# Kernel tuning notes

Hardware: AMD Instinct MI355X
Metric: run time of the kernel (lower is better)

The kernel has to match this reference:

```python
import jax, jax.numpy as jnp
import numpy as np

B, C, N, V, W = 2, 4, 224, 7, 256
EMB, H = 256, 4
TOKEN_DIM = C * N           # 896
HF = int(C * 2.66)          # 10 (GDFN hidden features)
EPS_LN = 1e-6


def _dwconv3(x, w):
    # depthwise 3x3, padding=1; x:[B,Ch,Hh,Ww], w:[Ch,1,3,3]
    return jax.lax.conv_general_dilated(
        x, w, window_strides=(1, 1), padding='SAME',
        feature_group_count=x.shape[1],
        dimension_numbers=('NCHW', 'OIHW', 'NCHW'))


def _layernorm_c(x, g, b):
    # LayerNorm over channel dim (NCHW), eps=1e-6
    m = jnp.mean(x, axis=1, keepdims=True)
    v = jnp.mean((x - m) ** 2, axis=1, keepdims=True)
    return (x - m) / jnp.sqrt(v + EPS_LN) * g[None, :, None, None] + b[None, :, None, None]


def setup_inputs() -> dict:
    key = jax.random.key(0)
    ks = jax.random.split(key, 12)
    s = 0.02
    return {
        'buffer':     jax.random.normal(ks[0], (B, C, N, V, W), jnp.float32),
        'w_in':       jax.random.normal(ks[1], (EMB, TOKEN_DIM), jnp.float32) * s,
        'temperature': jnp.ones((1, H, 1, 1), jnp.float32),
        'ln1_g':      jnp.ones((EMB,), jnp.float32),
        'ln1_b':      jnp.zeros((EMB,), jnp.float32),
        'w_qkv':      jax.random.normal(ks[2], (3 * EMB, EMB), jnp.float32) * s,
        'w_qkv_dw':   jax.random.normal(ks[3], (3 * EMB, 1, 3, 3), jnp.float32) * s,
        'w_proj':     jax.random.normal(ks[4], (TOKEN_DIM, EMB), jnp.float32) * s,
        'w_attca':    jax.random.normal(ks[5], (2 * H, H), jnp.float32) * s,
        'ln2_g':      jnp.ones((C,), jnp.float32),
        'ln2_b':      jnp.zeros((C,), jnp.float32),
        'w_pin':      jax.random.normal(ks[6], (2 * HF, C), jnp.float32) * s,
        'w_dw':       jax.random.normal(ks[7], (2 * HF, 1, 3, 3), jnp.float32) * s,
        'w_pout':     jax.random.normal(ks[8], (C, HF), jnp.float32) * s,
    }


def reference(buffer, w_in, temperature, ln1_g, ln1_b, w_qkv, w_qkv_dw,
              w_proj, w_attca, ln2_g, ln2_b, w_pin, w_dw, w_pout):
    S = V * W
    d = EMB // H
    # b c n v w -> b (v w) (c n)
    x_tok = buffer.transpose(0, 3, 4, 1, 2).reshape(B, S, C * N)
    # b c n v w -> (b n) c v w
    x_res = buffer.transpose(0, 2, 1, 3, 4).reshape(B * N, C, V, W)

    x_tok = jnp.einsum('bsk,ek->bse', x_tok, w_in)                  # linear_in
    x = x_tok.reshape(B, V, W, EMB).transpose(0, 3, 1, 2)           # b emb v w
    x_norm = _layernorm_c(x, ln1_g, ln1_b)

    qkv = jnp.einsum('bchw,oc->bohw', x_norm, w_qkv)                # 1x1 conv
    qkv = _dwconv3(qkv, w_qkv_dw)
    q, k, v_ = jnp.split(qkv, 3, axis=1)

    def heads(t):  # b (h d) v w -> b h (v w) d
        return t.reshape(B, H, d, S).transpose(0, 1, 3, 2)
    q, k, v_ = heads(q), heads(k), heads(v_)

    # F.normalize(dim=-1), eps=1e-12
    q = q / jnp.maximum(jnp.linalg.norm(q, axis=-1, keepdims=True), 1e-12)
    k = k / jnp.maximum(jnp.linalg.norm(k, axis=-1, keepdims=True), 1e-12)

    attn_logits = jnp.einsum('bhid,bhjd->bhij', q, k) * temperature
    attn0 = jax.nn.softmax(attn_logits, axis=-1)
    attn1 = jnp.maximum(attn_logits, 0.0) ** 2
    attn1 = jax.nn.gelu(attn1, approximate=False) * attn1
    x_att = jnp.einsum('bhij,oh->boij', attn1, w_attca)             # 1x1 conv over heads
    scale, shift = jnp.split(x_att, 2, axis=1)
    attn = attn0 * (1.0 + scale) + shift

    out = jnp.einsum('bhij,bhjd->bhid', attn, v_)
    out = out.transpose(0, 1, 3, 2).reshape(B, EMB, V, W)           # b (h d) v w
    out = jnp.einsum('bchw,oc->bohw', out, w_proj)                  # proj to token_dim
    out = out.reshape(B, C, N, V, W).transpose(0, 2, 1, 3, 4).reshape(B * N, C, V, W)

    x2 = x_res + out
    epi = _layernorm_c(x2, ln2_g, ln2_b)
    # GDFN
    h_ = jnp.einsum('bchw,oc->bohw', epi, w_pin)
    h_ = _dwconv3(h_, w_dw)
    h1, h2 = jnp.split(h_, 2, axis=1)
    h_ = jax.nn.gelu(h1, approximate=False) * h2
    epi = jnp.einsum('bchw,oc->bohw', h_, w_pout)
    epi = x2 + epi

    return epi.reshape(B, N, C, V, W).transpose(0, 2, 1, 3, 4)      # b c n v w
```

## Files before the change

kernel.cpp:

```cpp
#include <hip/hip_runtime.h>
#include <math.h>

#define B_ 2
#define C_ 4
#define N_ 224
#define V_ 7
#define W_ 256
#define S_ 1792
#define EMB_ 256
#define H_ 4
#define D_ 64
#define TOK_ 896
#define HF_ 10
#define JC_ 4
#define JRANGE_ (S_ / JC_)
#define JSTEPS_ (JRANGE_ / 32)

typedef __attribute__((ext_vector_type(8))) short short8;
typedef __attribute__((ext_vector_type(4))) short bf16x4;
typedef __attribute__((ext_vector_type(4))) float f32x4;

#define MFMA16(a, b, c) __builtin_amdgcn_mfma_f32_16x16x32_bf16(a, b, c, 0, 0, 0)

__device__ inline short f2bf(float f) {
    union { float f; unsigned u; } x; x.f = f;
    unsigned u = x.u;
    unsigned r = (u + 0x7fffu + ((u >> 16) & 1u)) >> 16;
    return (short)r;
}
__device__ inline float bf2f(short s) {
    union { unsigned u; float f; } x;
    x.u = ((unsigned)(unsigned short)s) << 16;
    return x.f;
}

__global__ __launch_bounds__(256) void gemm_mfma_kernel(
    const float* __restrict__ A, const float* __restrict__ Bact, float* __restrict__ Cm,
    int M, int N, int K, long b_bs, long c_bs)
{
    Bact += (long)blockIdx.z * b_bs;
    Cm   += (long)blockIdx.z * c_bs;
    const int m0 = blockIdx.y * 128, n0 = blockIdx.x * 128;
    __shared__ __align__(16) short As[128][40];
    __shared__ __align__(16) short Bs[128][40];
    const int t = threadIdx.x;
    const int lane = t & 63;
    const int wave = t >> 6;
    const int wr = wave >> 1, wc = wave & 1;
    const int col = lane & 15, grp = lane >> 4;
    const int ar = t >> 3, ak = (t & 7) * 4;
    const int bn = t & 127, kb = (t >> 7) * 16;
    f32x4 acc[4][4];
    #pragma unroll
    for (int i = 0; i < 4; ++i)
        #pragma unroll
        for (int j = 0; j < 4; ++j) acc[i][j] = (f32x4){0.f, 0.f, 0.f, 0.f};
    for (int k0 = 0; k0 < K; k0 += 32) {
        #pragma unroll
        for (int p = 0; p < 4; ++p) {
            f32x4 v = *(const f32x4*)&A[(long)(m0 + ar + p * 32) * K + k0 + ak];
            bf16x4 pk;
            pk[0] = f2bf(v[0]); pk[1] = f2bf(v[1]); pk[2] = f2bf(v[2]); pk[3] = f2bf(v[3]);
            *(bf16x4*)&As[ar + p * 32][ak] = pk;
        }
        float tv[16];
        #pragma unroll
        for (int j = 0; j < 16; ++j)
            tv[j] = Bact[(long)(k0 + kb + j) * N + n0 + bn];
        short8 b0, b1;
        #pragma unroll
        for (int j = 0; j < 8; ++j) { b0[j] = f2bf(tv[j]); b1[j] = f2bf(tv[8 + j]); }
        *(short8*)&Bs[bn][kb]     = b0;
        *(short8*)&Bs[bn][kb + 8] = b1;
        __syncthreads();
        short8 af[4], bfr[4];
        #pragma unroll
        for (int m16 = 0; m16 < 4; ++m16)
            af[m16] = *(const short8*)&As[wr * 64 + m16 * 16 + col][grp * 8];
        #pragma unroll
        for (int n16 = 0; n16 < 4; ++n16)
            bfr[n16] = *(const short8*)&Bs[wc * 64 + n16 * 16 + col][grp * 8];
        #pragma unroll
        for (int m16 = 0; m16 < 4; ++m16)
            #pragma unroll
            for (int n16 = 0; n16 < 4; ++n16)
                acc[m16][n16] = MFMA16(af[m16], bfr[n16], acc[m16][n16]);
        __syncthreads();
    }
    #pragma unroll
    for (int m16 = 0; m16 < 4; ++m16)
        #pragma unroll
        for (int n16 = 0; n16 < 4; ++n16)
            #pragma unroll
            for (int r = 0; r < 4; ++r)
                Cm[(long)(m0 + wr * 64 + m16 * 16 + grp * 4 + r) * N
                   + n0 + wc * 64 + n16 * 16 + col] = acc[m16][n16][r];
}

__global__ __launch_bounds__(256) void ln1_kernel(
    const float* __restrict__ X, const float* __restrict__ g,
    const float* __restrict__ b, float* __restrict__ Y)
{
    int sl = threadIdx.x & 63, dg = threadIdx.x >> 6;
    int s = blockIdx.x * 64 + sl;
    int img = blockIdx.y;
    const float* xp = X + (long)img * EMB_ * S_ + s;
    float sum = 0.f, sq = 0.f;
    for (int c = dg * 64; c < dg * 64 + 64; ++c) {
        float v = xp[(long)c * S_];
        sum += v; sq += v * v;
    }
    __shared__ float rs[64][5], rq[64][5];
    rs[sl][dg] = sum; rq[sl][dg] = sq;
    __syncthreads();
    float tot = rs[sl][0] + rs[sl][1] + rs[sl][2] + rs[sl][3];
    float tq  = rq[sl][0] + rq[sl][1] + rq[sl][2] + rq[sl][3];
    float mean = tot * (1.f / EMB_);
    float var  = tq * (1.f / EMB_) - mean * mean;
    float inv  = rsqrtf(var + 1e-6f);
    float* yp = Y + (long)img * EMB_ * S_ + s;
    for (int c = dg * 64; c < dg * 64 + 64; ++c)
        yp[(long)c * S_] = (xp[(long)c * S_] - mean) * inv * g[c] + b[c];
}

__global__ void dwconv3_kernel(const float* __restrict__ X, const float* __restrict__ Wt,
                               float* __restrict__ Y, short* __restrict__ vbf,
                               long total, int Ch)
{
    long idx = (long)blockIdx.x * blockDim.x + threadIdx.x;
    long stride = (long)gridDim.x * blockDim.x;
    for (; idx < total; idx += stride) {
        int w = (int)(idx % W_);
        long t = idx / W_;
        int h = (int)(t % V_); t /= V_;
        int ch = (int)(t % Ch);
        long img_ch = idx / ((long)V_ * W_);
        const float* wp = Wt + ch * 9;
        const float* xp = X + img_ch * (V_ * W_);
        float acc = 0.f;
        #pragma unroll
        for (int dy = -1; dy <= 1; ++dy) {
            int h2 = h + dy;
            if (h2 < 0 || h2 >= V_) continue;
            #pragma unroll
            for (int dx = -1; dx <= 1; ++dx) {
                int w2 = w + dx;
                if (w2 < 0 || w2 >= W_) continue;
                acc += xp[h2 * W_ + w2] * wp[(dy + 1) * 3 + (dx + 1)];
            }
        }
        Y[idx] = acc;
        if (vbf && ch >= 512) {
            int b = (int)(t / Ch);
            vbf[((long)b * 256 + (ch - 512)) * S_ + h * W_ + w] = f2bf(acc);
        }
    }
}

__global__ __launch_bounds__(256) void headnorm_kernel(
    const float* __restrict__ qkvd, const float* __restrict__ temp,
    short* __restrict__ qn, short* __restrict__ kn)
{
    int s0 = blockIdx.x * 64;
    int bh = blockIdx.y; int b = bh >> 2, h = bh & 3;
    int isq = blockIdx.z;
    int ch0 = b * 768 + (isq ? 0 : EMB_) + h * 64;
    short* dst = (isq ? qn : kn) + (long)bh * S_ * 64;
    __shared__ float tile[64][65];
    __shared__ float red[64][4];
    int t = threadIdx.x;
    int sl = t & 63, dg = t >> 6;
    float part = 0.f;
    for (int dd = 0; dd < 16; ++dd) {
        int d = dg * 16 + dd;
        float v = qkvd[(long)(ch0 + d) * S_ + s0 + sl];
        tile[sl][d] = v;
        part += v * v;
    }
    red[sl][dg] = part;
    __syncthreads();
    int d = t & 63, sg = t >> 6;
    float tmul = isq ? temp[h] : 1.f;
    for (int si = 0; si < 16; ++si) {
        int s = sg * 16 + si;
        float nrm = sqrtf(red[s][0] + red[s][1] + red[s][2] + red[s][3]);
        float scale = tmul / fmaxf(nrm, 1e-12f);
        dst[(long)(s0 + s) * 64 + d] = f2bf(tile[s][d] * scale);
    }
}

__global__ __launch_bounds__(256) void attn_kernel(
    const short* __restrict__ qn, const short* __restrict__ kn,
    const short* __restrict__ vbf, const float* __restrict__ wat,
    float* __restrict__ partY, float* __restrict__ partZ)
{
    int h = threadIdx.x >> 6;
    int lane = threadIdx.x & 63;
    int col = lane & 15, grp = lane >> 4;
    int itile = blockIdx.x;
    int jc = blockIdx.y;
    int b = blockIdx.z;
    int ibase = itile * 16;
    int bh = b * 4 + h;

    const short* qrow = qn + ((long)bh * S_ + ibase + col) * 64 + grp * 8;
    short8 qa0 = *(const short8*)qrow;
    short8 qa1 = *(const short8*)(qrow + 32);
    float wsc[4], wsh[4];
    #pragma unroll
    for (int hh = 0; hh < 4; ++hh) { wsc[hh] = wat[h * 4 + hh]; wsh[hh] = wat[(4 + h) * 4 + hh]; }

    __shared__ __align__(16) float exch[4][16][33];
    __shared__ __align__(16) short pbuf[4][2][16][40];

    f32x4 y1[4], y2[4];
    #pragma unroll
    for (int ds = 0; ds < 4; ++ds) {
        y1[ds] = (f32x4){0.f, 0.f, 0.f, 0.f};
        y2[ds] = (f32x4){0.f, 0.f, 0.f, 0.f};
    }
    float zp[4] = {0.f, 0.f, 0.f, 0.f};
    const short* kbase = kn + (long)bh * S_ * 64;
    const short* vbase = vbf + ((long)b * 256 + h * 64) * S_;

    for (int jt = 0; jt < JSTEPS_; ++jt) {
        int jbase = jc * JRANGE_ + jt * 32;
        f32x4 lf[2];
        #pragma unroll
        for (int js = 0; js < 2; ++js) {
            const short* krow = kbase + (long)(jbase + js * 16 + col) * 64 + grp * 8;
            short8 kb0 = *(const short8*)krow;
            short8 kb1 = *(const short8*)(krow + 32);
            f32x4 a = (f32x4){0.f, 0.f, 0.f, 0.f};
            a = MFMA16(qa0, kb0, a);
            a = MFMA16(qa1, kb1, a);
            lf[js] = a;
        }
        float a1own[8];
        #pragma unroll
        for (int js = 0; js < 2; ++js)
            #pragma unroll
            for (int r = 0; r < 4; ++r) {
                float l = lf[js][r];
                float rr = fmaxf(l, 0.f);
                float s1 = rr * rr;
                float a1 = s1 * 0.5f * (1.f + erff(s1 * 0.70710678118654752f)) * s1;
                a1own[js * 4 + r] = a1;
                exch[h][grp * 4 + r][js * 16 + col] = a1;
            }
        __syncthreads();
        #pragma unroll
        for (int js = 0; js < 2; ++js)
            #pragma unroll
            for (int r = 0; r < 4; ++r) {
                float sc = 0.f, sh = 0.f;
                #pragma unroll
                for (int hh = 0; hh < 4; ++hh) {
                    float a1v = (hh == h) ? a1own[js * 4 + r]
                                          : exch[hh][grp * 4 + r][js * 16 + col];
                    sc += a1v * wsc[hh];
                    sh += a1v * wsh[hh];
                }
                float e = __expf(lf[js][r]);
                zp[r] += e;
                pbuf[h][0][grp * 4 + r][js * 16 + col] = f2bf(e * (1.f + sc));
                pbuf[h][1][grp * 4 + r][js * 16 + col] = f2bf(sh);
            }
        __syncthreads();
        short8 p1a = *(const short8*)&pbuf[h][0][col][grp * 8];
        short8 p2a = *(const short8*)&pbuf[h][1][col][grp * 8];
        #pragma unroll
        for (int ds = 0; ds < 4; ++ds) {
            const short* vrow = vbase + (long)(ds * 16 + col) * S_ + jbase + grp * 8;
            short8 vb = *(const short8*)vrow;
            y1[ds] = MFMA16(p1a, vb, y1[ds]);
            y2[ds] = MFMA16(p2a, vb, y2[ds]);
        }
    }

    #pragma unroll
    for (int o = 1; o < 16; o <<= 1) {
        #pragma unroll
        for (int r = 0; r < 4; ++r) zp[r] += __shfl_xor(zp[r], o, 64);
    }
    if (col == 0) {
        #pragma unroll
        for (int r = 0; r < 4; ++r)
            partZ[((long)(jc * 2 + b) * 4 + h) * S_ + ibase + grp * 4 + r] = zp[r];
    }
    float* tb = &exch[h][0][0];
    long ybase = ((((long)jc * 2 + b) * 4 + h) * 2) * 64 * S_;
    for (int acc = 0; acc < 2; ++acc) {
        #pragma unroll
        for (int ds = 0; ds < 4; ++ds) {
            f32x4 y = acc ? y2[ds] : y1[ds];
            #pragma unroll
            for (int r = 0; r < 4; ++r) tb[col * 17 + grp * 4 + r] = y[r];
            #pragma unroll
            for (int p = 0; p < 4; ++p) {
                float val = tb[(p * 4 + grp) * 17 + col];
                partY[ybase + ((long)acc * 64 + ds * 16 + p * 4 + grp) * S_ + ibase + col] = val;
            }
        }
    }
}

__global__ __launch_bounds__(256) void combine_kernel(
    const float* __restrict__ partY, const float* __restrict__ partZ,
    float* __restrict__ outav)
{
    int idx = blockIdx.x * 256 + threadIdx.x;
    int i = idx % S_;
    int t = idx / S_;
    int d = t & 63; t >>= 6;
    int h = t & 3; int b = t >> 2;
    float y1 = 0.f, y2 = 0.f, z = 0.f;
    #pragma unroll
    for (int jc = 0; jc < JC_; ++jc) {
        long base = ((((long)jc * 2 + b) * 4 + h) * 2) * 64 * S_;
        y1 += partY[base + (long)d * S_ + i];
        y2 += partY[base + (long)(64 + d) * S_ + i];
        z  += partZ[((long)(jc * 2 + b) * 4 + h) * S_ + i];
    }
    outav[((long)b * 256 + h * 64 + d) * S_ + i] = y1 / z + y2;
}

__global__ __launch_bounds__(256) void resid_pin_kernel(
    const float* __restrict__ buffer, const float* __restrict__ proj,
    const float* __restrict__ g2, const float* __restrict__ b2,
    const float* __restrict__ w_pin,
    float* __restrict__ x2, short* __restrict__ hbuf)
{
    int s = blockIdx.x * 256 + threadIdx.x;
    int bn = blockIdx.y;
    int b = bn / N_, n = bn % N_;
    float v[4];
    float sum = 0.f;
    #pragma unroll
    for (int c = 0; c < 4; ++c) {
        float xr = buffer[((long)(b * 4 + c) * N_ + n) * S_ + s];
        float pr = proj[((long)b * TOK_ + c * N_ + n) * S_ + s];
        v[c] = xr + pr;
        x2[((long)bn * 4 + c) * S_ + s] = v[c];
        sum += v[c];
    }
    float mean = sum * 0.25f;
    float var = 0.f;
    #pragma unroll
    for (int c = 0; c < 4; ++c) { float dd = v[c] - mean; var += dd * dd; }
    var *= 0.25f;
    float inv = rsqrtf(var + 1e-6f);
    float e[4];
    #pragma unroll
    for (int c = 0; c < 4; ++c) e[c] = (v[c] - mean) * inv * g2[c] + b2[c];
    for (int o = 0; o < 2 * HF_; ++o) {
        float a = 0.f;
        #pragma unroll
        for (int c = 0; c < 4; ++c) a += w_pin[o * 4 + c] * e[c];
        hbuf[((long)bn * (2 * HF_) + o) * S_ + s] = f2bf(a);
    }
}

__global__ __launch_bounds__(448) void gdfn_kernel(
    const short* __restrict__ hbuf, const float* __restrict__ w_dw,
    const float* __restrict__ w_pout, const float* __restrict__ x2,
    float* __restrict__ out)
{
    int xt = blockIdx.x;
    int bn = blockIdx.y;
    int b = bn / N_, n = bn % N_;
    int x0 = xt * 64;
    __shared__ float tile[20][7][66];
    int tid = threadIdx.x;
    for (int idx = tid; idx < 20 * 7 * 66; idx += 448) {
        int ch = idx / (7 * 66); int rem = idx % (7 * 66);
        int y = rem / 66; int xx = rem % 66;
        int gx = x0 + xx - 1;
        float v = 0.f;
        if (gx >= 0 && gx < W_) v = bf2f(hbuf[((long)bn * 20 + ch) * S_ + y * W_ + gx]);
        tile[ch][y][xx] = v;
    }
    __syncthreads();
    int y = tid / 64, x = tid & 63;
    float hd[20];
    #pragma unroll
    for (int ch = 0; ch < 20; ++ch) {
        const float* wp = w_dw + ch * 9;
        float acc = 0.f;
        #pragma unroll
        for (int dy = -1; dy <= 1; ++dy) {
            int yy = y + dy;
            if (yy < 0 || yy >= V_) continue;
            #pragma unroll
            for (int dx = -1; dx <= 1; ++dx)
                acc += tile[ch][yy][x + 1 + dx] * wp[(dy + 1) * 3 + (dx + 1)];
        }
        hd[ch] = acc;
    }
    float g[HF_];
    #pragma unroll
    for (int f = 0; f < HF_; ++f) {
        float h1 = hd[f];
        g[f] = 0.5f * h1 * (1.f + erff(h1 * 0.70710678118654752f)) * hd[HF_ + f];
    }
    int s = y * W_ + x0 + x;
    #pragma unroll
    for (int c = 0; c < 4; ++c) {
        float a = 0.f;
        #pragma unroll
        for (int f = 0; f < HF_; ++f) a += w_pout[c * HF_ + f] * g[f];
        out[((long)(b * 4 + c) * N_ + n) * S_ + s] = x2[((long)bn * 4 + c) * S_ + s] + a;
    }
}

extern "C" void kernel_launch(void* const* d_in, const int* in_sizes, int n_in,
                              void* d_out, int out_size, void* d_ws, size_t ws_size,
                              hipStream_t stream)
{
    const float* buffer = (const float*)d_in[0];
    const float* w_in   = (const float*)d_in[1];
    const float* temp   = (const float*)d_in[2];
    const float* ln1_g  = (const float*)d_in[3];
    const float* ln1_b  = (const float*)d_in[4];
    const float* w_qkv  = (const float*)d_in[5];
    const float* w_qkv_dw = (const float*)d_in[6];
    const float* w_proj = (const float*)d_in[7];
    const float* w_attca = (const float*)d_in[8];
    const float* ln2_g  = (const float*)d_in[9];
    const float* ln2_b  = (const float*)d_in[10];
    const float* w_pin  = (const float*)d_in[11];
    const float* w_dw   = (const float*)d_in[12];
    const float* w_pout = (const float*)d_in[13];
    float* out = (float*)d_out;

    float* ws = (float*)d_ws;
    float* qkvd    = ws;
    short* qn      = (short*)(ws + 2752512);
    short* kn      = (short*)(ws + 3211264);
    short* vbf     = (short*)(ws + 3670016);
    float* partY   = ws + 4128768;
    float* partZ   = ws + 11468800;
    float* outav   = ws + 11526144;
    float* xw      = ws + 12443648;
    float* xn      = ws + 13361152;
    float* qkv     = ws + 14278656;
    float* outproj = ws + 17031168;
    float* x2      = ws + 20242432;
    short* hbuf    = (short*)(ws + 23453696);

    gemm_mfma_kernel<<<dim3(14, 2, 2), 256, 0, stream>>>(
        w_in, buffer, xw, EMB_, S_, TOK_, (long)TOK_ * S_, (long)EMB_ * S_);

    ln1_kernel<<<dim3(28, 2), 256, 0, stream>>>(xw, ln1_g, ln1_b, xn);

    gemm_mfma_kernel<<<dim3(14, 6, 2), 256, 0, stream>>>(
        w_qkv, xn, qkv, 3 * EMB_, S_, EMB_, (long)EMB_ * S_, (long)3 * EMB_ * S_);

    {
        long total = (long)B_ * 3 * EMB_ * S_;
        dwconv3_kernel<<<(int)((total + 255) / 256), 256, 0, stream>>>(
            qkv, w_qkv_dw, qkvd, vbf, total, 3 * EMB_);
    }

    headnorm_kernel<<<dim3(28, 8, 2), 256, 0, stream>>>(qkvd, temp, qn, kn);

    attn_kernel<<<dim3(112, JC_, B_), 256, 0, stream>>>(qn, kn, vbf, w_attca, partY, partZ);

    combine_kernel<<<3584, 256, 0, stream>>>(partY, partZ, outav);

    gemm_mfma_kernel<<<dim3(14, 7, 2), 256, 0, stream>>>(
        w_proj, outav, outproj, TOK_, S_, EMB_, (long)EMB_ * S_, (long)TOK_ * S_);

    resid_pin_kernel<<<dim3(7, B_ * N_), 256, 0, stream>>>(
        buffer, outproj, ln2_g, ln2_b, w_pin, x2, hbuf);

    gdfn_kernel<<<dim3(4, B_ * N_), 448, 0, stream>>>(hbuf, w_dw, w_pout, x2, out);
}
```

Measured before the change: 228.4 us.

## Shrink GEMM tiles with swizzled LDS, fuse LN1 into QKV GEMM, rework attention

GEMMs move from 128x128 tiles to 64x64 tiles with XOR-swizzled shared memory, giving more blocks on these small problems. LayerNorm1 now only computes per-column statistics, and the normalisation is applied while the QKV GEMM loads its B operand, which removes the normalised intermediate buffer. The attention kernel doubles the j-split (JC 8), swaps MFMA operand order so probabilities stay in registers instead of going through a shared buffer, and replaces erf GELU with a tanh/sigmoid approximation. The approximate GELU may change numerics, and the larger split doubles partial-result traffic in the combine step.

Result: slower. 237.2 us (+3.9%).

```diff
diff --git a/kernel.cpp b/kernel.cpp
--- a/kernel.cpp
+++ b/kernel.cpp
@@ -12,12 +12,11 @@
 #define D_ 64
 #define TOK_ 896
 #define HF_ 10
-#define JC_ 4
+#define JC_ 8
 #define JRANGE_ (S_ / JC_)
 #define JSTEPS_ (JRANGE_ / 32)
 
 typedef __attribute__((ext_vector_type(8))) short short8;
-typedef __attribute__((ext_vector_type(4))) short bf16x4;
 typedef __attribute__((ext_vector_type(4))) float f32x4;
 
 #define MFMA16(a, b, c) __builtin_amdgcn_mfma_f32_16x16x32_bf16(a, b, c, 0, 0, 0)
@@ -34,72 +33,80 @@
     return x.f;
 }
 
-__global__ __launch_bounds__(256) void gemm_mfma_kernel(
+__global__ __launch_bounds__(256) void gemm64_kernel(
     const float* __restrict__ A, const float* __restrict__ Bact, float* __restrict__ Cm,
-    int M, int N, int K, long b_bs, long c_bs)
-{
-    Bact += (long)blockIdx.z * b_bs;
-    Cm   += (long)blockIdx.z * c_bs;
-    const int m0 = blockIdx.y * 128, n0 = blockIdx.x * 128;
-    __shared__ __align__(16) short As[128][40];
-    __shared__ __align__(16) short Bs[128][40];
+    int M, int N, int K, long b_bs, long c_bs,
+    const float* __restrict__ mu, const float* __restrict__ ri,
+    const float* __restrict__ lg, const float* __restrict__ lb)
+{
+    const int bz = blockIdx.z;
+    Bact += (long)bz * b_bs;
+    Cm   += (long)bz * c_bs;
+    const int m0 = blockIdx.y * 64, n0 = blockIdx.x * 64;
+    __shared__ __align__(16) short As[64 * 32];
+    __shared__ __align__(16) short Bs[64 * 32];
     const int t = threadIdx.x;
-    const int lane = t & 63;
-    const int wave = t >> 6;
+    const int lane = t & 63, wave = t >> 6;
     const int wr = wave >> 1, wc = wave & 1;
     const int col = lane & 15, grp = lane >> 4;
-    const int ar = t >> 3, ak = (t & 7) * 4;
-    const int bn = t & 127, kb = (t >> 7) * 16;
-    f32x4 acc[4][4];
-    #pragma unroll
-    for (int i = 0; i < 4; ++i)
-        #pragma unroll
-        for (int j = 0; j < 4; ++j) acc[i][j] = (f32x4){0.f, 0.f, 0.f, 0.f};
+    const int s_row = t >> 2, s_ch = t & 3;
+    const int bn = t & 63, bkc = t >> 6;
+    float mun = 0.f, rin = 1.f;
+    if (mu) { mun = mu[(long)bz * N + n0 + bn]; rin = ri[(long)bz * N + n0 + bn]; }
+    f32x4 acc[2][2];
+    #pragma unroll
+    for (int i = 0; i < 2; ++i)
+        #pragma unroll
+        for (int j = 0; j < 2; ++j) acc[i][j] = (f32x4){0.f, 0.f, 0.f, 0.f};
     for (int k0 = 0; k0 < K; k0 += 32) {
-        #pragma unroll
-        for (int p = 0; p < 4; ++p) {
-            f32x4 v = *(const f32x4*)&A[(long)(m0 + ar + p * 32) * K + k0 + ak];
-            bf16x4 pk;
-            pk[0] = f2bf(v[0]); pk[1] = f2bf(v[1]); pk[2] = f2bf(v[2]); pk[3] = f2bf(v[3]);
-            *(bf16x4*)&As[ar + p * 32][ak] = pk;
-        }
-        float tv[16];
-        #pragma unroll
-        for (int j = 0; j < 16; ++j)
-            tv[j] = Bact[(long)(k0 + kb + j) * N + n0 + bn];
-        short8 b0, b1;
-        #pragma unroll
-        for (int j = 0; j < 8; ++j) { b0[j] = f2bf(tv[j]); b1[j] = f2bf(tv[8 + j]); }
-        *(short8*)&Bs[bn][kb]     = b0;
-        *(short8*)&Bs[bn][kb + 8] = b1;
+        const float* ap = &A[(long)(m0 + s_row) * K + k0 + s_ch * 8];
+        f32x4 a0 = *(const f32x4*)ap;
+        f32x4 a1 = *(const f32x4*)(ap + 4);
+        short8 av;
+        av[0] = f2bf(a0[0]); av[1] = f2bf(a0[1]); av[2] = f2bf(a0[2]); av[3] = f2bf(a0[3]);
+        av[4] = f2bf(a1[0]); av[5] = f2bf(a1[1]); av[6] = f2bf(a1[2]); av[7] = f2bf(a1[3]);
+        int abyte = (s_row << 6) + (s_ch << 4);
+        *(short8*)((char*)As + (abyte ^ ((s_row & 7) << 4))) = av;
+        short8 bw;
+        #pragma unroll
+        for (int j = 0; j < 8; ++j) {
+            float v = Bact[(long)(k0 + bkc * 8 + j) * N + n0 + bn];
+            if (mu) v = fmaf((v - mun) * rin, lg[k0 + bkc * 8 + j], lb[k0 + bkc * 8 + j]);
+            bw[j] = f2bf(v);
+        }
+        int bbyte = (bn << 6) + (bkc << 4);
+        *(short8*)((char*)Bs + (bbyte ^ ((bn & 7) << 4))) = bw;
         __syncthreads();
-        short8 af[4], bfr[4];
-        #pragma unroll
-        for (int m16 = 0; m16 < 4; ++m16)
-            af[m16] = *(const short8*)&As[wr * 64 + m16 * 16 + col][grp * 8];
-        #pragma unroll
-        for (int n16 = 0; n16 < 4; ++n16)
-            bfr[n16] = *(const short8*)&Bs[wc * 64 + n16 * 16 + col][grp * 8];
-        #pragma unroll
-        for (int m16 = 0; m16 < 4; ++m16)
-            #pragma unroll
-            for (int n16 = 0; n16 < 4; ++n16)
-                acc[m16][n16] = MFMA16(af[m16], bfr[n16], acc[m16][n16]);
+        short8 af[2], bfv[2];
+        #pragma unroll
+        for (int mm = 0; mm < 2; ++mm) {
+            int r = wr * 32 + mm * 16 + col;
+            af[mm] = *(const short8*)((const char*)As + ((((r) << 6) + (grp << 4)) ^ ((r & 7) << 4)));
+        }
+        #pragma unroll
+        for (int nn = 0; nn < 2; ++nn) {
+            int r = wc * 32 + nn * 16 + col;
+            bfv[nn] = *(const short8*)((const char*)Bs + ((((r) << 6) + (grp << 4)) ^ ((r & 7) << 4)));
+        }
+        #pragma unroll
+        for (int mm = 0; mm < 2; ++mm)
+            #pragma unroll
+            for (int nn = 0; nn < 2; ++nn)
+                acc[mm][nn] = MFMA16(af[mm], bfv[nn], acc[mm][nn]);
         __syncthreads();
     }
     #pragma unroll
-    for (int m16 = 0; m16 < 4; ++m16)
-        #pragma unroll
-        for (int n16 = 0; n16 < 4; ++n16)
+    for (int mm = 0; mm < 2; ++mm)
+        #pragma unroll
+        for (int nn = 0; nn < 2; ++nn)
             #pragma unroll
             for (int r = 0; r < 4; ++r)
-                Cm[(long)(m0 + wr * 64 + m16 * 16 + grp * 4 + r) * N
-                   + n0 + wc * 64 + n16 * 16 + col] = acc[m16][n16][r];
-}
-
-__global__ __launch_bounds__(256) void ln1_kernel(
-    const float* __restrict__ X, const float* __restrict__ g,
-    const float* __restrict__ b, float* __restrict__ Y)
+                Cm[(long)(m0 + wr * 32 + mm * 16 + grp * 4 + r) * N
+                   + n0 + wc * 32 + nn * 16 + col] = acc[mm][nn][r];
+}
+
+__global__ __launch_bounds__(256) void ln1stats_kernel(
+    const float* __restrict__ X, float* __restrict__ mu, float* __restrict__ ri)
 {
     int sl = threadIdx.x & 63, dg = threadIdx.x >> 6;
     int s = blockIdx.x * 64 + sl;
@@ -113,14 +120,14 @@
     __shared__ float rs[64][5], rq[64][5];
     rs[sl][dg] = sum; rq[sl][dg] = sq;
     __syncthreads();
-    float tot = rs[sl][0] + rs[sl][1] + rs[sl][2] + rs[sl][3];
-    float tq  = rq[sl][0] + rq[sl][1] + rq[sl][2] + rq[sl][3];
-    float mean = tot * (1.f / EMB_);
-    float var  = tq * (1.f / EMB_) - mean * mean;
-    float inv  = rsqrtf(var + 1e-6f);
-    float* yp = Y + (long)img * EMB_ * S_ + s;
-    for (int c = dg * 64; c < dg * 64 + 64; ++c)
-        yp[(long)c * S_] = (xp[(long)c * S_] - mean) * inv * g[c] + b[c];
+    if (dg == 0) {
+        float tot = rs[sl][0] + rs[sl][1] + rs[sl][2] + rs[sl][3];
+        float tq  = rq[sl][0] + rq[sl][1] + rq[sl][2] + rq[sl][3];
+        float mean = tot * (1.f / EMB_);
+        float var  = tq * (1.f / EMB_) - mean * mean;
+        mu[(long)img * S_ + s] = mean;
+        ri[(long)img * S_ + s] = rsqrtf(var + 1e-6f);
+    }
 }
 
 __global__ void dwconv3_kernel(const float* __restrict__ X, const float* __restrict__ Wt,
@@ -194,14 +201,14 @@
     const short* __restrict__ vbf, const float* __restrict__ wat,
     float* __restrict__ partY, float* __restrict__ partZ)
 {
-    int h = threadIdx.x >> 6;
-    int lane = threadIdx.x & 63;
-    int col = lane & 15, grp = lane >> 4;
-    int itile = blockIdx.x;
-    int jc = blockIdx.y;
-    int b = blockIdx.z;
-    int ibase = itile * 16;
-    int bh = b * 4 + h;
+    const int h = threadIdx.x >> 6;
+    const int lane = threadIdx.x & 63;
+    const int col = lane & 15, grp = lane >> 4;
+    const int itile = blockIdx.x;
+    const int jc = blockIdx.y;
+    const int b = blockIdx.z;
+    const int ibase = itile * 16;
+    const int bh = b * 4 + h;
 
     const short* qrow = qn + ((long)bh * S_ + ibase + col) * 64 + grp * 8;
     short8 qa0 = *(const short8*)qrow;
@@ -210,96 +217,94 @@
     #pragma unroll
     for (int hh = 0; hh < 4; ++hh) { wsc[hh] = wat[h * 4 + hh]; wsh[hh] = wat[(4 + h) * 4 + hh]; }
 
-    __shared__ __align__(16) float exch[4][16][33];
-    __shared__ __align__(16) short pbuf[4][2][16][40];
+    __shared__ float exch[4][32][34];
 
     f32x4 y1[4], y2[4];
     #pragma unroll
-    for (int ds = 0; ds < 4; ++ds) {
-        y1[ds] = (f32x4){0.f, 0.f, 0.f, 0.f};
-        y2[ds] = (f32x4){0.f, 0.f, 0.f, 0.f};
-    }
-    float zp[4] = {0.f, 0.f, 0.f, 0.f};
+    for (int dt = 0; dt < 4; ++dt) {
+        y1[dt] = (f32x4){0.f, 0.f, 0.f, 0.f};
+        y2[dt] = (f32x4){0.f, 0.f, 0.f, 0.f};
+    }
+    float z = 0.f;
     const short* kbase = kn + (long)bh * S_ * 64;
     const short* vbase = vbf + ((long)b * 256 + h * 64) * S_;
+    const int joffA = (col & 3) + 8 * (col >> 2);
 
     for (int jt = 0; jt < JSTEPS_; ++jt) {
         int jbase = jc * JRANGE_ + jt * 32;
         f32x4 lf[2];
         #pragma unroll
-        for (int js = 0; js < 2; ++js) {
-            const short* krow = kbase + (long)(jbase + js * 16 + col) * 64 + grp * 8;
-            short8 kb0 = *(const short8*)krow;
-            short8 kb1 = *(const short8*)(krow + 32);
+        for (int tt = 0; tt < 2; ++tt) {
+            const short* krow = kbase + (long)(jbase + joffA + 4 * tt) * 64 + grp * 8;
+            short8 ka0 = *(const short8*)krow;
+            short8 ka1 = *(const short8*)(krow + 32);
             f32x4 a = (f32x4){0.f, 0.f, 0.f, 0.f};
-            a = MFMA16(qa0, kb0, a);
-            a = MFMA16(qa1, kb1, a);
-            lf[js] = a;
-        }
-        float a1own[8];
-        #pragma unroll
-        for (int js = 0; js < 2; ++js)
+            a = MFMA16(ka0, qa0, a);
+            a = MFMA16(ka1, qa1, a);
+            lf[tt] = a;
+        }
+        float a1own[2][4], ee[2][4];
+        #pragma unroll
+        for (int tt = 0; tt < 2; ++tt)
             #pragma unroll
             for (int r = 0; r < 4; ++r) {
-                float l = lf[js][r];
+                float l = lf[tt][r];
                 float rr = fmaxf(l, 0.f);
                 float s1 = rr * rr;
-                float a1 = s1 * 0.5f * (1.f + erff(s1 * 0.70710678118654752f)) * s1;
-                a1own[js * 4 + r] = a1;
-                exch[h][grp * 4 + r][js * 16 + col] = a1;
+                float u = fmaf(s1 * s1, 0.0713548162726f * s1, 1.59576912161f * s1);
+                float sg = __builtin_amdgcn_rcpf(1.f + __expf(-u));
+                float a1 = s1 * sg * s1;
+                a1own[tt][r] = a1;
+                ee[tt][r] = __expf(l);
+                exch[h][r + 4 * tt + 8 * grp][col] = a1;
             }
         __syncthreads();
-        #pragma unroll
-        for (int js = 0; js < 2; ++js)
+        short8 pa, pb;
+        #pragma unroll
+        for (int tt = 0; tt < 2; ++tt)
             #pragma unroll
             for (int r = 0; r < 4; ++r) {
+                int jloc = r + 4 * tt + 8 * grp;
                 float sc = 0.f, sh = 0.f;
                 #pragma unroll
                 for (int hh = 0; hh < 4; ++hh) {
-                    float a1v = (hh == h) ? a1own[js * 4 + r]
-                                          : exch[hh][grp * 4 + r][js * 16 + col];
+                    float a1v = (hh == h) ? a1own[tt][r] : exch[hh][jloc][col];
                     sc += a1v * wsc[hh];
                     sh += a1v * wsh[hh];
                 }
-                float e = __expf(lf[js][r]);
-                zp[r] += e;
-                pbuf[h][0][grp * 4 + r][js * 16 + col] = f2bf(e * (1.f + sc));
-                pbuf[h][1][grp * 4 + r][js * 16 + col] = f2bf(sh);
+                float e = ee[tt][r];
+                z += e;
+                pa[tt * 4 + r] = f2bf(e * (1.f + sc));
+                pb[tt * 4 + r] = f2bf(sh);
             }
         __syncthreads();
-        short8 p1a = *(const short8*)&pbuf[h][0][col][grp * 8];
-        short8 p2a = *(const short8*)&pbuf[h][1][col][grp * 8];
-        #pragma unroll
-        for (int ds = 0; ds < 4; ++ds) {
-            const short* vrow = vbase + (long)(ds * 16 + col) * S_ + jbase + grp * 8;
+        #pragma unroll
+        for (int dt = 0; dt < 4; ++dt) {
+            const short* vrow = vbase + (long)(dt * 16 + col) * S_ + jbase + grp * 8;
             short8 vb = *(const short8*)vrow;
-            y1[ds] = MFMA16(p1a, vb, y1[ds]);
-            y2[ds] = MFMA16(p2a, vb, y2[ds]);
-        }
-    }
-
-    #pragma unroll
-    for (int o = 1; o < 16; o <<= 1) {
-        #pragma unroll
-        for (int r = 0; r < 4; ++r) zp[r] += __shfl_xor(zp[r], o, 64);
-    }
-    if (col == 0) {
-        #pragma unroll
-        for (int r = 0; r < 4; ++r)
-            partZ[((long)(jc * 2 + b) * 4 + h) * S_ + ibase + grp * 4 + r] = zp[r];
-    }
+            y1[dt] = MFMA16(pa, vb, y1[dt]);
+            y2[dt] = MFMA16(pb, vb, y2[dt]);
+        }
+    }
+
+    z += __shfl_xor(z, 16, 64);
+    z += __shfl_xor(z, 32, 64);
+    if (grp == 0)
+        partZ[((long)(jc * 2 + b) * 4 + h) * S_ + ibase + col] = z;
+
+    __syncthreads();
     float* tb = &exch[h][0][0];
     long ybase = ((((long)jc * 2 + b) * 4 + h) * 2) * 64 * S_;
     for (int acc = 0; acc < 2; ++acc) {
         #pragma unroll
-        for (int ds = 0; ds < 4; ++ds) {
-            f32x4 y = acc ? y2[ds] : y1[ds];
-            #pragma unroll
-            for (int r = 0; r < 4; ++r) tb[col * 17 + grp * 4 + r] = y[r];
+        for (int dt = 0; dt < 4; ++dt) {
+            f32x4 y = acc ? y2[dt] : y1[dt];
+            #pragma unroll
+            for (int r = 0; r < 4; ++r) tb[(grp * 4 + r) * 17 + col] = y[r];
             #pragma unroll
             for (int p = 0; p < 4; ++p) {
-                float val = tb[(p * 4 + grp) * 17 + col];
-                partY[ybase + ((long)acc * 64 + ds * 16 + p * 4 + grp) * S_ + ibase + col] = val;
+                float val = tb[col * 17 + p * 4 + grp];
+                partY[ybase + ((long)acc * 64 + dt * 16 + p * 4 + grp) * S_ + ibase + col] = val;
             }
         }
     }
@@ -439,22 +444,25 @@
     short* kn      = (short*)(ws + 3211264);
     short* vbf     = (short*)(ws + 3670016);
     float* partY   = ws + 4128768;
-    float* partZ   = ws + 11468800;
-    float* outav   = ws + 11526144;
-    float* xw      = ws + 12443648;
-    float* xn      = ws + 13361152;
-    float* qkv     = ws + 14278656;
-    float* outproj = ws + 17031168;
-    float* x2      = ws + 20242432;
-    short* hbuf    = (short*)(ws + 23453696);
-
-    gemm_mfma_kernel<<<dim3(14, 2, 2), 256, 0, stream>>>(
-        w_in, buffer, xw, EMB_, S_, TOK_, (long)TOK_ * S_, (long)EMB_ * S_);
-
-    ln1_kernel<<<dim3(28, 2), 256, 0, stream>>>(xw, ln1_g, ln1_b, xn);
-
-    gemm_mfma_kernel<<<dim3(14, 6, 2), 256, 0, stream>>>(
-        w_qkv, xn, qkv, 3 * EMB_, S_, EMB_, (long)EMB_ * S_, (long)3 * EMB_ * S_);
+    float* partZ   = ws + 18808832;
+    float* outav   = ws + 18923520;
+    float* xw      = ws + 19841024;
+    float* mu      = ws + 20758528;
+    float* ri      = ws + 20762112;
+    float* qkv     = ws + 20765696;
+    float* outproj = ws + 23518208;
+    float* x2      = ws + 26729472;
+    short* hbuf    = (short*)(ws + 29940736);
+
+    gemm64_kernel<<<dim3(28, 4, 2), 256, 0, stream>>>(
+        w_in, buffer, xw, EMB_, S_, TOK_, (long)TOK_ * S_, (long)EMB_ * S_,
+        nullptr, nullptr, nullptr, nullptr);
+
+    ln1stats_kernel<<<dim3(28, 2), 256, 0, stream>>>(xw, mu, ri);
+
+    gemm64_kernel<<<dim3(28, 12, 2), 256, 0, stream>>>(
+        w_qkv, xw, qkv, 3 * EMB_, S_, EMB_, (long)EMB_ * S_, (long)3 * EMB_ * S_,
+        mu, ri, ln1_g, ln1_b);
 
     {
         long total = (long)B_ * 3 * EMB_ * S_;
@@ -468,8 +476,9 @@
 
     combine_kernel<<<3584, 256, 0, stream>>>(partY, partZ, outav);
 
-    gemm_mfma_kernel<<<dim3(14, 7, 2), 256, 0, stream>>>(
-        w_proj, outav, outproj, TOK_, S_, EMB_, (long)EMB_ * S_, (long)TOK_ * S_);
+    gemm64_kernel<<<dim3(28, 14, 2), 256, 0, stream>>>(
+        w_proj, outav, outproj, TOK_, S_, EMB_, (long)EMB_ * S_, (long)TOK_ * S_,
+        nullptr, nullptr, nullptr, nullptr);
 
     resid_pin_kernel<<<dim3(7, B_ * N_), 256, 0, stream>>>(
         buffer, outproj, ln2_g, ln2_b, w_pin, x2, hbuf);
```
